# Kernel optimization log

Hardware: AMD Instinct MI355X
Metric: run time of the kernel (lower is better)

The kernel has to match this reference:

```python
import jax, jax.numpy as jnp
import numpy as np

TEMPERATURE = 0.1


def setup_inputs() -> dict:
    key = jax.random.key(0)
    k1, k2 = jax.random.split(key)
    N, D = 8192, 512
    embeddings = jax.random.normal(k1, (N, D), dtype=jnp.float32)
    labels = jax.random.randint(k2, (N,), 0, 16, dtype=jnp.int64)
    return {"embeddings": embeddings, "labels": labels}


def reference(embeddings, labels):
    # Vectorized SupCon: for each anchor i,
    #   +mean over positives j!=i of s_ij  -  logsumexp over all j!=i of s_ij
    # where s_ij = <e_i, e_j> / T. Final loss = -sum_i(...) / N * T.
    N = embeddings.shape[0]
    T = TEMPERATURE
    S = jnp.einsum('id,jd->ij', embeddings, embeddings) / T  # [N, N]
    eye = jnp.eye(N, dtype=bool)
    pos_mask = (labels[:, None] == labels[None, :]) & (~eye)  # positives, self excluded
    pos_counts = jnp.sum(pos_mask, axis=1)  # [N], assumed > 0 (every class has >=2 samples)
    pos_term = jnp.sum(jnp.where(pos_mask, S, 0.0), axis=1) / pos_counts
    neg_inf = jnp.array(-jnp.inf, dtype=S.dtype)
    lse = jax.nn.logsumexp(jnp.where(eye, neg_inf, S), axis=1)  # over j != i
    loss = jnp.sum(pos_term - lse)
    return -loss / N * T
```

## Files before the change

kernel.cpp:

```cpp
#include <hip/hip_runtime.h>
#include <stdint.h>

#define NROWS 8192
#define DIM   512
#define NPART 128

typedef __attribute__((ext_vector_type(8))) short short8;
typedef __attribute__((ext_vector_type(4))) float f32x4;
typedef unsigned int u32;

#define OFF_EBF   0u
#define OFF_X     8388608u
#define OFF_PM    8388608u
#define OFF_PL    12582912u
#define OFF_CLS   16777216u
#define OFF_CNT   16809984u
#define OFF_NRM   16810048u
#define OFF_BLK   16842816u

__device__ __forceinline__ void gload16(const void* g, void* l) {
  __builtin_amdgcn_global_load_lds((const __attribute__((address_space(1))) u32*)g,
                                   (__attribute__((address_space(3))) u32*)l, 16, 0, 0);
}

__device__ __forceinline__ unsigned short f2bf(float f) {
  u32 u = __float_as_uint(f);
  u32 r = (u + 0x7fffu + ((u >> 16) & 1u)) >> 16;
  return (unsigned short)r;
}

__global__ __launch_bounds__(256) void k_prep(const float* __restrict__ E,
                                              unsigned short* __restrict__ Ebf,
                                              float* __restrict__ nrm) {
  const int tid = threadIdx.x;
  const int lane = tid & 63;
  const int wid = tid >> 6;
  const int row = blockIdx.x * 4 + wid;
  const float4* src = (const float4*)(E + row * DIM + lane * 8);
  float4 v0 = src[0], v1 = src[1];
  float ns = v0.x*v0.x + v0.y*v0.y + v0.z*v0.z + v0.w*v0.w
           + v1.x*v1.x + v1.y*v1.y + v1.z*v1.z + v1.w*v1.w;
  u32 p0 = (u32)f2bf(v0.x) | ((u32)f2bf(v0.y) << 16);
  u32 p1 = (u32)f2bf(v0.z) | ((u32)f2bf(v0.w) << 16);
  u32 p2 = (u32)f2bf(v1.x) | ((u32)f2bf(v1.y) << 16);
  u32 p3 = (u32)f2bf(v1.z) | ((u32)f2bf(v1.w) << 16);
  *(uint4*)(Ebf + row * DIM + lane * 8) = make_uint4(p0, p1, p2, p3);
  #pragma unroll
  for (int s = 1; s < 64; s <<= 1) ns += __shfl_xor(ns, s);
  if (lane == 0) nrm[row] = ns;
}

__global__ __launch_bounds__(256) void k_cls(const float* __restrict__ E,
                                             const int* __restrict__ lab,
                                             float* __restrict__ Cpart,
                                             int* __restrict__ cnt) {
  __shared__ int lcnt[16];
  const int t = threadIdx.x;
  const int b = blockIdx.x;
  const int i0 = b * 32;
  if (t < 16) lcnt[t] = 0;
  __syncthreads();
  if (t < 32) atomicAdd(&lcnt[lab[i0 + t]], 1);
  float a0[16], a1[16];
  #pragma unroll
  for (int c = 0; c < 16; ++c) { a0[c] = 0.f; a1[c] = 0.f; }
  #pragma unroll 8
  for (int r = 0; r < 32; ++r) {
    const int lbl = lab[i0 + r];
    const float2 v = *(const float2*)(E + (i0 + r) * DIM + t * 2);
    #pragma unroll
    for (int c = 0; c < 16; ++c) {
      a0[c] += (c == lbl) ? v.x : 0.f;
      a1[c] += (c == lbl) ? v.y : 0.f;
    }
  }
  #pragma unroll
  for (int c = 0; c < 16; ++c)
    *(float2*)(Cpart + b * 8192 + c * DIM + t * 2) = make_float2(a0[c], a1[c]);
  __syncthreads();
  if (t < 16) atomicAdd(&cnt[t], lcnt[t]);
}

__global__ __launch_bounds__(256) void k_clsred(const float* __restrict__ Cpart,
                                                float* __restrict__ Cls) {
  const int idx = blockIdx.x * 256 + threadIdx.x;
  float s = 0.f;
  #pragma unroll 8
  for (int b = 0; b < 256; ++b) s += Cpart[b * 8192 + idx];
  Cls[idx] = s;
}

__global__ __launch_bounds__(256) void k_main(const unsigned short* __restrict__ Ebf,
                                              float* __restrict__ partM,
                                              float* __restrict__ partL) {
  const int jt = blockIdx.x;
  const int it = blockIdx.y;
  if (it > jt) return;

  __shared__ __align__(16) unsigned short As[128 * 64];
  __shared__ __align__(16) unsigned short Bs[128 * 64];

  const int tid  = threadIdx.x;
  const int lane = tid & 63;
  const int wid  = tid >> 6;
  const int wm   = wid >> 1;
  const int wn   = wid & 1;
  const int g    = lane >> 4;
  const int l15  = lane & 15;

  const int i0 = it * 128;
  const int j0 = jt * 128;

  const float C2 = 14.4269504088896f;

  int srow[4], selem[4];
  #pragma unroll
  for (int r = 0; r < 4; ++r) {
    const int D   = r * 4096 + tid * 16;
    const int row = D >> 7;
    const int cb  = (D >> 4) & 7;
    const int cs  = cb ^ (row & 7);
    srow[r]  = row;
    selem[r] = cs * 8;
  }

  f32x4 acc[4][4];
  #pragma unroll
  for (int a = 0; a < 4; ++a)
    #pragma unroll
    for (int b = 0; b < 4; ++b) {
      f32x4 z = {0.f, 0.f, 0.f, 0.f};
      acc[a][b] = z;
    }

  for (int kc = 0; kc < 8; ++kc) {
    #pragma unroll
    for (int r = 0; r < 4; ++r) {
      gload16(Ebf + (i0 + srow[r]) * DIM + kc * 64 + selem[r], &As[r * 2048 + tid * 8]);
      gload16(Ebf + (j0 + srow[r]) * DIM + kc * 64 + selem[r], &Bs[r * 2048 + tid * 8]);
    }
    __syncthreads();

    #pragma unroll
    for (int ks = 0; ks < 2; ++ks) {
      const int x = ((ks << 2) | g) ^ (l15 & 7);
      short8 av[4], bv[4];
      #pragma unroll
      for (int mf = 0; mf < 4; ++mf)
        av[mf] = *(const short8*)&As[(wm * 64 + mf * 16 + l15) * 64 + x * 8];
      #pragma unroll
      for (int nf = 0; nf < 4; ++nf)
        bv[nf] = *(const short8*)&Bs[(wn * 64 + nf * 16 + l15) * 64 + x * 8];
      #pragma unroll
      for (int mf = 0; mf < 4; ++mf)
        #pragma unroll
        for (int nf = 0; nf < 4; ++nf)
          acc[mf][nf] = __builtin_amdgcn_mfma_f32_16x16x32_bf16(av[mf], bv[nf], acc[mf][nf], 0, 0, 0);
    }
    __syncthreads();
  }

  const bool diagt = (it == jt);

  #pragma unroll
  for (int mf = 0; mf < 4; ++mf) {
    #pragma unroll
    for (int reg = 0; reg < 4; ++reg) {
      float v0 = acc[mf][0][reg];
      float v1 = acc[mf][1][reg];
      float v2 = acc[mf][2][reg];
      float v3 = acc[mf][3][reg];
      if (diagt) {
        const int rloc  = wm * 64 + mf * 16 + g * 4 + reg;
        const int cbase = wn * 64 + l15;
        v0 = (rloc == cbase)      ? -1e30f : v0;
        v1 = (rloc == cbase + 16) ? -1e30f : v1;
        v2 = (rloc == cbase + 32) ? -1e30f : v2;
        v3 = (rloc == cbase + 48) ? -1e30f : v3;
      }
      float m = fmaxf(fmaxf(v0, v1), fmaxf(v2, v3)) * C2;
      #pragma unroll
      for (int s = 1; s < 16; s <<= 1) m = fmaxf(m, __shfl_xor(m, s));
      float p = exp2f(__builtin_fmaf(v0, C2, -m)) + exp2f(__builtin_fmaf(v1, C2, -m))
              + exp2f(__builtin_fmaf(v2, C2, -m)) + exp2f(__builtin_fmaf(v3, C2, -m));
      #pragma unroll
      for (int s = 1; s < 16; s <<= 1) p += __shfl_xor(p, s);
      if (l15 == 0) {
        const int row = i0 + wm * 64 + mf * 16 + g * 4 + reg;
        partM[row * NPART + jt * 2 + wn] = m;
        partL[row * NPART + jt * 2 + wn] = p;
      }
    }
  }

  if (!diagt) {
    #pragma unroll
    for (int nf = 0; nf < 4; ++nf) {
      float m = -1e30f;
      #pragma unroll
      for (int mf = 0; mf < 4; ++mf)
        #pragma unroll
        for (int reg = 0; reg < 4; ++reg) m = fmaxf(m, acc[mf][nf][reg]);
      m *= C2;
      m = fmaxf(m, __shfl_xor(m, 16));
      m = fmaxf(m, __shfl_xor(m, 32));
      float p = 0.f;
      #pragma unroll
      for (int mf = 0; mf < 4; ++mf)
        #pragma unroll
        for (int reg = 0; reg < 4; ++reg)
          p += exp2f(__builtin_fmaf(acc[mf][nf][reg], C2, -m));
      p += __shfl_xor(p, 16);
      p += __shfl_xor(p, 32);
      if (g == 0) {
        const int row = j0 + wn * 64 + nf * 16 + l15;
        partM[row * NPART + it * 2 + wm] = m;
        partL[row * NPART + it * 2 + wm] = p;
      }
    }
  }
}

__global__ __launch_bounds__(256) void k_merge(const int* __restrict__ lab,
                                               const float* __restrict__ nrm,
                                               const float* __restrict__ partM,
                                               const float* __restrict__ partL,
                                               const int* __restrict__ cnt,
                                               float* __restrict__ blkout) {
  __shared__ float red[4];
  const int tid = threadIdx.x;
  const int lane = tid & 63;
  const int wid = tid >> 6;
  const int row = blockIdx.x * 4 + wid;

  float m1 = partM[row * NPART + lane];
  float l1 = partL[row * NPART + lane];
  const float m2 = partM[row * NPART + 64 + lane];
  const float l2 = partL[row * NPART + 64 + lane];
  float m = fmaxf(m1, m2);
  float l = l1 * exp2f(m1 - m) + l2 * exp2f(m2 - m);
  #pragma unroll
  for (int s = 1; s < 64; s <<= 1) {
    const float mo = __shfl_xor(m, s);
    const float lo = __shfl_xor(l, s);
    const float mn = fmaxf(m, mo);
    l = l * exp2f(m - mn) + lo * exp2f(mo - mn);
    m = mn;
  }
  if (lane == 0) {
    const float lse = 0.6931471805599453f * (m + log2f(l));
    const int lbl = lab[row];
    const float pc = (float)(cnt[lbl] - 1);
    red[wid] = -nrm[row] * 10.0f / pc - lse;
  }
  __syncthreads();
  if (tid == 0) blkout[blockIdx.x] = red[0] + red[1] + red[2] + red[3];
}

__global__ __launch_bounds__(256) void k_final(const float* __restrict__ blkout,
                                               const float* __restrict__ Cls,
                                               const int* __restrict__ cnt,
                                               float* __restrict__ out) {
  __shared__ float w[4];
  const int t = threadIdx.x;
  float s = 0.f;
  #pragma unroll
  for (int k = 0; k < 8; ++k) s += blkout[t + 256 * k];
  #pragma unroll
  for (int c = 0; c < 16; ++c) {
    const float2 v = *(const float2*)(Cls + c * DIM + t * 2);
    const float wc = 10.0f / (float)(cnt[c] - 1);
    s += wc * (v.x * v.x + v.y * v.y);
  }
  #pragma unroll
  for (int sh = 1; sh < 64; sh <<= 1) s += __shfl_xor(s, sh);
  if ((t & 63) == 0) w[t >> 6] = s;
  __syncthreads();
  if (t == 0) out[0] = (w[0] + w[1] + w[2] + w[3]) * (-0.1f / 8192.0f);
}

extern "C" void kernel_launch(void* const* d_in, const int* in_sizes, int n_in,
                              void* d_out, int out_size, void* d_ws, size_t ws_size,
                              hipStream_t stream) {
  (void)in_sizes; (void)n_in; (void)out_size; (void)ws_size;
  const float* E  = (const float*)d_in[0];
  const int* lab  = (const int*)d_in[1];
  char* ws = (char*)d_ws;
  unsigned short* Ebf = (unsigned short*)(ws + OFF_EBF);
  float* Cprt = (float*)(ws + OFF_X);
  float* pM   = (float*)(ws + OFF_PM);
  float* pL   = (float*)(ws + OFF_PL);
  float* Cls  = (float*)(ws + OFF_CLS);
  int*   cnt  = (int*)  (ws + OFF_CNT);
  float* nrm  = (float*)(ws + OFF_NRM);
  float* blk  = (float*)(ws + OFF_BLK);

  hipMemsetAsync(ws + OFF_CNT, 0, 64, stream);

  k_prep  <<<NROWS / 4, 256, 0, stream>>>(E, Ebf, nrm);
  k_cls   <<<256, 256, 0, stream>>>(E, lab, Cprt, cnt);
  k_clsred<<<32, 256, 0, stream>>>(Cprt, Cls);
  dim3 grid(64, 64);
  k_main  <<<grid, 256, 0, stream>>>(Ebf, pM, pL);
  k_merge <<<NROWS / 4, 256, 0, stream>>>(lab, nrm, pM, pL, cnt, blk);
  k_final <<<1, 256, 0, stream>>>(blk, Cls, cnt, (float*)d_out);
}
```

Measured before the change: 208.9 us.

## Drop LDS staging in GEMM, compact triangular grid, use LDS atomics for class sums

The main Gram kernel no longer stages tiles in LDS. Each wave loads its bf16 fragments straight from global memory into registers, which removes the barriers and LDS traffic. The 64x64 grid, where half the blocks exited early, becomes a 65x32 grid that maps onto the upper triangle of tiles exactly, so no launched block is wasted. The class-sum kernel now accumulates in shared memory with atomics over 64 rows per block and launches half as many partial blocks. The trade-off is that operand reuse now depends on L1/L2 caching instead of LDS, and uncoalesced direct loads with LDS atomic contention may cost more than they save.

```diff
diff --git a/kernel.cpp b/kernel.cpp
--- a/kernel.cpp
+++ b/kernel.cpp
@@ -17,11 +17,6 @@
 #define OFF_CNT   16809984u
 #define OFF_NRM   16810048u
 #define OFF_BLK   16842816u
-
-__device__ __forceinline__ void gload16(const void* g, void* l) {
-  __builtin_amdgcn_global_load_lds((const __attribute__((address_space(1))) u32*)g,
-                                   (__attribute__((address_space(3))) u32*)l, 16, 0, 0);
-}
 
 __device__ __forceinline__ unsigned short f2bf(float f) {
   u32 u = __float_as_uint(f);
@@ -54,30 +49,23 @@
                                              const int* __restrict__ lab,
                                              float* __restrict__ Cpart,
                                              int* __restrict__ cnt) {
+  __shared__ float lcls[16 * DIM];
   __shared__ int lcnt[16];
   const int t = threadIdx.x;
   const int b = blockIdx.x;
-  const int i0 = b * 32;
+  const int i0 = b * 64;
+  for (int k = t; k < 16 * DIM; k += 256) lcls[k] = 0.f;
   if (t < 16) lcnt[t] = 0;
   __syncthreads();
-  if (t < 32) atomicAdd(&lcnt[lab[i0 + t]], 1);
-  float a0[16], a1[16];
-  #pragma unroll
-  for (int c = 0; c < 16; ++c) { a0[c] = 0.f; a1[c] = 0.f; }
-  #pragma unroll 8
-  for (int r = 0; r < 32; ++r) {
+  if (t < 64) atomicAdd(&lcnt[lab[i0 + t]], 1);
+  for (int r = 0; r < 64; ++r) {
     const int lbl = lab[i0 + r];
     const float2 v = *(const float2*)(E + (i0 + r) * DIM + t * 2);
-    #pragma unroll
-    for (int c = 0; c < 16; ++c) {
-      a0[c] += (c == lbl) ? v.x : 0.f;
-      a1[c] += (c == lbl) ? v.y : 0.f;
-    }
-  }
-  #pragma unroll
-  for (int c = 0; c < 16; ++c)
-    *(float2*)(Cpart + b * 8192 + c * DIM + t * 2) = make_float2(a0[c], a1[c]);
-  __syncthreads();
+    atomicAdd(&lcls[lbl * DIM + t * 2],     v.x);
+    atomicAdd(&lcls[lbl * DIM + t * 2 + 1], v.y);
+  }
+  __syncthreads();
+  for (int k = t; k < 16 * DIM; k += 256) Cpart[b * 8192 + k] = lcls[k];
   if (t < 16) atomicAdd(&cnt[t], lcnt[t]);
 }
 
@@ -86,19 +74,18 @@
   const int idx = blockIdx.x * 256 + threadIdx.x;
   float s = 0.f;
   #pragma unroll 8
-  for (int b = 0; b < 256; ++b) s += Cpart[b * 8192 + idx];
+  for (int b = 0; b < 128; ++b) s += Cpart[b * 8192 + idx];
   Cls[idx] = s;
 }
 
 __global__ __launch_bounds__(256) void k_main(const unsigned short* __restrict__ Ebf,
                                               float* __restrict__ partM,
                                               float* __restrict__ partL) {
-  const int jt = blockIdx.x;
-  const int it = blockIdx.y;
-  if (it > jt) return;
-
-  __shared__ __align__(16) unsigned short As[128 * 64];
-  __shared__ __align__(16) unsigned short Bs[128 * 64];
+  const int x = blockIdx.x;
+  const int y = blockIdx.y;
+  int IT, JT;
+  if (x < 64 - y) { IT = y;      JT = y + x; }
+  else            { IT = 63 - y; JT = x - 1; }
 
   const int tid  = threadIdx.x;
   const int lane = tid & 63;
@@ -108,59 +95,58 @@
   const int g    = lane >> 4;
   const int l15  = lane & 15;
 
-  const int i0 = it * 128;
-  const int j0 = jt * 128;
+  const int a = IT * 2 + wm;
+  const int b = JT * 2 + wn;
+  const bool diagblk = (IT == JT);
+  const bool diag64  = (a == b);
 
   const float C2 = 14.4269504088896f;
 
-  int srow[4], selem[4];
-  #pragma unroll
-  for (int r = 0; r < 4; ++r) {
-    const int D   = r * 4096 + tid * 16;
-    const int row = D >> 7;
-    const int cb  = (D >> 4) & 7;
-    const int cs  = cb ^ (row & 7);
-    srow[r]  = row;
-    selem[r] = cs * 8;
-  }
+  const unsigned short* pa0 = Ebf + (a * 64 + l15) * DIM + g * 8;
+  const unsigned short* pb0 = Ebf + (b * 64 + l15) * DIM + g * 8;
+  const unsigned short* pa1 = pa0 + 16 * DIM;
+  const unsigned short* pa2 = pa0 + 32 * DIM;
+  const unsigned short* pa3 = pa0 + 48 * DIM;
+  const unsigned short* pb1 = pb0 + 16 * DIM;
+  const unsigned short* pb2 = pb0 + 32 * DIM;
+  const unsigned short* pb3 = pb0 + 48 * DIM;
 
   f32x4 acc[4][4];
   #pragma unroll
-  for (int a = 0; a < 4; ++a)
+  for (int i = 0; i < 4; ++i)
     #pragma unroll
-    for (int b = 0; b < 4; ++b) {
+    for (int j = 0; j < 4; ++j) {
       f32x4 z = {0.f, 0.f, 0.f, 0.f};
-      acc[a][b] = z;
+      acc[i][j] = z;
     }
 
-  for (int kc = 0; kc < 8; ++kc) {
-    #pragma unroll
-    for (int r = 0; r < 4; ++r) {
-      gload16(Ebf + (i0 + srow[r]) * DIM + kc * 64 + selem[r], &As[r * 2048 + tid * 8]);
-      gload16(Ebf + (j0 + srow[r]) * DIM + kc * 64 + selem[r], &Bs[r * 2048 + tid * 8]);
-    }
-    __syncthreads();
-
-    #pragma unroll
-    for (int ks = 0; ks < 2; ++ks) {
-      const int x = ((ks << 2) | g) ^ (l15 & 7);
-      short8 av[4], bv[4];
-      #pragma unroll
-      for (int mf = 0; mf < 4; ++mf)
-        av[mf] = *(const short8*)&As[(wm * 64 + mf * 16 + l15) * 64 + x * 8];
-      #pragma unroll
-      for (int nf = 0; nf < 4; ++nf)
-        bv[nf] = *(const short8*)&Bs[(wn * 64 + nf * 16 + l15) * 64 + x * 8];
-      #pragma unroll
-      for (int mf = 0; mf < 4; ++mf)
-        #pragma unroll
-        for (int nf = 0; nf < 4; ++nf)
-          acc[mf][nf] = __builtin_amdgcn_mfma_f32_16x16x32_bf16(av[mf], bv[nf], acc[mf][nf], 0, 0, 0);
-    }
-    __syncthreads();
-  }
-
-  const bool diagt = (it == jt);
+  #pragma unroll 4
+  for (int ks = 0; ks < 16; ++ks) {
+    short8 av0 = *(const short8*)(pa0 + ks * 32);
+    short8 av1 = *(const short8*)(pa1 + ks * 32);
+    short8 av2 = *(const short8*)(pa2 + ks * 32);
+    short8 av3 = *(const short8*)(pa3 + ks * 32);
+    short8 bv0 = *(const short8*)(pb0 + ks * 32);
+    short8 bv1 = *(const short8*)(pb1 + ks * 32);
+    short8 bv2 = *(const short8*)(pb2 + ks * 32);
+    short8 bv3 = *(const short8*)(pb3 + ks * 32);
+    acc[0][0] = __builtin_amdgcn_mfma_f32_16x16x32_bf16(av0, bv0, acc[0][0], 0, 0, 0);
+    acc[0][1] = __builtin_amdgcn_mfma_f32_16x16x32_bf16(av0, bv1, acc[0][1], 0, 0, 0);
+    acc[0][2] = __builtin_amdgcn_mfma_f32_16x16x32_bf16(av0, bv2, acc[0][2], 0, 0, 0);
+    acc[0][3] = __builtin_amdgcn_mfma_f32_16x16x32_bf16(av0, bv3, acc[0][3], 0, 0, 0);
+    acc[1][0] = __builtin_amdgcn_mfma_f32_16x16x32_bf16(av1, bv0, acc[1][0], 0, 0, 0);
+    acc[1][1] = __builtin_amdgcn_mfma_f32_16x16x32_bf16(av1, bv1, acc[1][1], 0, 0, 0);
+    acc[1][2] = __builtin_amdgcn_mfma_f32_16x16x32_bf16(av1, bv2, acc[1][2], 0, 0, 0);
+    acc[1][3] = __builtin_amdgcn_mfma_f32_16x16x32_bf16(av1, bv3, acc[1][3], 0, 0, 0);
+    acc[2][0] = __builtin_amdgcn_mfma_f32_16x16x32_bf16(av2, bv0, acc[2][0], 0, 0, 0);
+    acc[2][1] = __builtin_amdgcn_mfma_f32_16x16x32_bf16(av2, bv1, acc[2][1], 0, 0, 0);
+    acc[2][2] = __builtin_amdgcn_mfma_f32_16x16x32_bf16(av2, bv2, acc[2][2], 0, 0, 0);
+    acc[2][3] = __builtin_amdgcn_mfma_f32_16x16x32_bf16(av2, bv3, acc[2][3], 0, 0, 0);
+    acc[3][0] = __builtin_amdgcn_mfma_f32_16x16x32_bf16(av3, bv0, acc[3][0], 0, 0, 0);
+    acc[3][1] = __builtin_amdgcn_mfma_f32_16x16x32_bf16(av3, bv1, acc[3][1], 0, 0, 0);
+    acc[3][2] = __builtin_amdgcn_mfma_f32_16x16x32_bf16(av3, bv2, acc[3][2], 0, 0, 0);
+    acc[3][3] = __builtin_amdgcn_mfma_f32_16x16x32_bf16(av3, bv3, acc[3][3], 0, 0, 0);
+  }
 
   #pragma unroll
   for (int mf = 0; mf < 4; ++mf) {
@@ -170,13 +156,12 @@
       float v1 = acc[mf][1][reg];
       float v2 = acc[mf][2][reg];
       float v3 = acc[mf][3][reg];
-      if (diagt) {
-        const int rloc  = wm * 64 + mf * 16 + g * 4 + reg;
-        const int cbase = wn * 64 + l15;
-        v0 = (rloc == cbase)      ? -1e30f : v0;
-        v1 = (rloc == cbase + 16) ? -1e30f : v1;
-        v2 = (rloc == cbase + 32) ? -1e30f : v2;
-        v3 = (rloc == cbase + 48) ? -1e30f : v3;
+      if (diag64) {
+        const int rloc = mf * 16 + g * 4 + reg;
+        v0 = (rloc == l15)      ? -1e30f : v0;
+        v1 = (rloc == 16 + l15) ? -1e30f : v1;
+        v2 = (rloc == 32 + l15) ? -1e30f : v2;
+        v3 = (rloc == 48 + l15) ? -1e30f : v3;
       }
       float m = fmaxf(fmaxf(v0, v1), fmaxf(v2, v3)) * C2;
       #pragma unroll
@@ -186,14 +171,14 @@
       #pragma unroll
       for (int s = 1; s < 16; s <<= 1) p += __shfl_xor(p, s);
       if (l15 == 0) {
-        const int row = i0 + wm * 64 + mf * 16 + g * 4 + reg;
-        partM[row * NPART + jt * 2 + wn] = m;
-        partL[row * NPART + jt * 2 + wn] = p;
+        const int row = a * 64 + mf * 16 + g * 4 + reg;
+        partM[row * NPART + b] = m;
+        partL[row * NPART + b] = p;
       }
     }
   }
 
-  if (!diagt) {
+  if (!diagblk) {
     #pragma unroll
     for (int nf = 0; nf < 4; ++nf) {
       float m = -1e30f;
@@ -213,9 +198,9 @@
       p += __shfl_xor(p, 16);
       p += __shfl_xor(p, 32);
       if (g == 0) {
-        const int row = j0 + wn * 64 + nf * 16 + l15;
-        partM[row * NPART + it * 2 + wm] = m;
-        partL[row * NPART + it * 2 + wm] = p;
+        const int row = b * 64 + nf * 16 + l15;
+        partM[row * NPART + a] = m;
+        partL[row * NPART + a] = p;
       }
     }
   }
@@ -298,9 +283,9 @@
   hipMemsetAsync(ws + OFF_CNT, 0, 64, stream);
 
   k_prep  <<<NROWS / 4, 256, 0, stream>>>(E, Ebf, nrm);
-  k_cls   <<<256, 256, 0, stream>>>(E, lab, Cprt, cnt);
+  k_cls   <<<128, 256, 0, stream>>>(E, lab, Cprt, cnt);
   k_clsred<<<32, 256, 0, stream>>>(Cprt, Cls);
-  dim3 grid(64, 64);
+  dim3 grid(65, 32);
   k_main  <<<grid, 256, 0, stream>>>(Ebf, pM, pL);
   k_merge <<<NROWS / 4, 256, 0, stream>>>(lab, nrm, pM, pL, cnt, blk);
   k_final <<<1, 256, 0, stream>>>(blk, Cls, cnt, (float*)d_out);
```

Measured after the change: 289.8 us. 1.39x slower.

## Balance triangular tile schedule in main kernel and build class sums from bf16

Applied to the files above, without the earlier changes.

The main kernel used to launch a full 64x64 grid and return early from the lower-triangle blocks. It now launches 1024 blocks. Each block walks a folded pair of triangle rows, so every block handles two or three tiles, which balances work and removes the idle launches. Separately, the class-sum kernel now reads the bf16 copy and accumulates with LDS float atomics instead of register select chains. That halves the global reads but lowers class-sum precision to bf16 and adds atomic contention in shared memory.

```diff
diff --git a/kernel.cpp b/kernel.cpp
--- a/kernel.cpp
+++ b/kernel.cpp
@@ -50,34 +50,27 @@
   if (lane == 0) nrm[row] = ns;
 }
 
-__global__ __launch_bounds__(256) void k_cls(const float* __restrict__ E,
+__global__ __launch_bounds__(256) void k_cls(const unsigned short* __restrict__ Ebf,
                                              const int* __restrict__ lab,
                                              float* __restrict__ Cpart,
                                              int* __restrict__ cnt) {
+  __shared__ float lcls[16 * DIM];
   __shared__ int lcnt[16];
   const int t = threadIdx.x;
   const int b = blockIdx.x;
   const int i0 = b * 32;
+  for (int k = t; k < 16 * DIM; k += 256) lcls[k] = 0.f;
   if (t < 16) lcnt[t] = 0;
   __syncthreads();
   if (t < 32) atomicAdd(&lcnt[lab[i0 + t]], 1);
-  float a0[16], a1[16];
-  #pragma unroll
-  for (int c = 0; c < 16; ++c) { a0[c] = 0.f; a1[c] = 0.f; }
-  #pragma unroll 8
   for (int r = 0; r < 32; ++r) {
     const int lbl = lab[i0 + r];
-    const float2 v = *(const float2*)(E + (i0 + r) * DIM + t * 2);
-    #pragma unroll
-    for (int c = 0; c < 16; ++c) {
-      a0[c] += (c == lbl) ? v.x : 0.f;
-      a1[c] += (c == lbl) ? v.y : 0.f;
-    }
-  }
-  #pragma unroll
-  for (int c = 0; c < 16; ++c)
-    *(float2*)(Cpart + b * 8192 + c * DIM + t * 2) = make_float2(a0[c], a1[c]);
+    const ushort2 v = *(const ushort2*)(Ebf + (i0 + r) * DIM + t * 2);
+    atomicAdd(&lcls[lbl * DIM + t * 2],     __uint_as_float((u32)v.x << 16));
+    atomicAdd(&lcls[lbl * DIM + t * 2 + 1], __uint_as_float((u32)v.y << 16));
+  }
   __syncthreads();
+  for (int k = t; k < 16 * DIM; k += 256) Cpart[b * 8192 + k] = lcls[k];
   if (t < 16) atomicAdd(&cnt[t], lcnt[t]);
 }
 
@@ -93,12 +86,14 @@
 __global__ __launch_bounds__(256) void k_main(const unsigned short* __restrict__ Ebf,
                                               float* __restrict__ partM,
                                               float* __restrict__ partL) {
-  const int jt = blockIdx.x;
-  const int it = blockIdx.y;
-  if (it > jt) return;
-
   __shared__ __align__(16) unsigned short As[128 * 64];
   __shared__ __align__(16) unsigned short Bs[128 * 64];
+
+  const int bid = blockIdx.x;
+  const int p = bid & 31;
+  const int c = bid >> 5;
+  const int nq  = (c == 0) ? 3 : 2;
+  const int off = (c == 0) ? 0 : (2 * c + 1);
 
   const int tid  = threadIdx.x;
   const int lane = tid & 63;
@@ -108,9 +103,6 @@
   const int g    = lane >> 4;
   const int l15  = lane & 15;
 
-  const int i0 = it * 128;
-  const int j0 = jt * 128;
-
   const float C2 = 14.4269504088896f;
 
   int srow[4], selem[4];
@@ -124,98 +116,106 @@
     selem[r] = cs * 8;
   }
 
-  f32x4 acc[4][4];
-  #pragma unroll
-  for (int a = 0; a < 4; ++a)
+  for (int qq = 0; qq < nq; ++qq) {
+    const int q = off + qq;
+    const int len1 = 64 - p;
+    const int it = (q < len1) ? p : 63 - p;
+    const int jt = (q < len1) ? p + q : (63 - p) + (q - len1);
+    const int i0 = it * 128;
+    const int j0 = jt * 128;
+    const bool diagt = (it == jt);
+
+    f32x4 acc[4][4];
     #pragma unroll
-    for (int b = 0; b < 4; ++b) {
-      f32x4 z = {0.f, 0.f, 0.f, 0.f};
-      acc[a][b] = z;
+    for (int a = 0; a < 4; ++a)
+      #pragma unroll
+      for (int b = 0; b < 4; ++b) {
+        f32x4 z = {0.f, 0.f, 0.f, 0.f};
+        acc[a][b] = z;
+      }
+
+    for (int kc = 0; kc < 8; ++kc) {
+      #pragma unroll
+      for (int r = 0; r < 4; ++r) {
+        gload16(Ebf + (i0 + srow[r]) * DIM + kc * 64 + selem[r], &As[r * 2048 + tid * 8]);
+        gload16(Ebf + (j0 + srow[r]) * DIM + kc * 64 + selem[r], &Bs[r * 2048 + tid * 8]);
+      }
+      __syncthreads();
+
+      #pragma unroll
+      for (int ks = 0; ks < 2; ++ks) {
+        const int x = ((ks << 2) | g) ^ (l15 & 7);
+        short8 av[4], bv[4];
+        #pragma unroll
+        for (int mf = 0; mf < 4; ++mf)
+          av[mf] = *(const short8*)&As[(wm * 64 + mf * 16 + l15) * 64 + x * 8];
+        #pragma unroll
+        for (int nf = 0; nf < 4; ++nf)
+          bv[nf] = *(const short8*)&Bs[(wn * 64 + nf * 16 + l15) * 64 + x * 8];
+        #pragma unroll
+        for (int mf = 0; mf < 4; ++mf)
+          #pragma unroll
+          for (int nf = 0; nf < 4; ++nf)
+            acc[mf][nf] = __builtin_amdgcn_mfma_f32_16x16x32_bf16(av[mf], bv[nf], acc[mf][nf], 0, 0, 0);
+      }
+      __syncthreads();
     }
 
-  for (int kc = 0; kc < 8; ++kc) {
     #pragma unroll
-    for (int r = 0; r < 4; ++r) {
-      gload16(Ebf + (i0 + srow[r]) * DIM + kc * 64 + selem[r], &As[r * 2048 + tid * 8]);
-      gload16(Ebf + (j0 + srow[r]) * DIM + kc * 64 + selem[r], &Bs[r * 2048 + tid * 8]);
+    for (int mf = 0; mf < 4; ++mf) {
+      #pragma unroll
+      for (int reg = 0; reg < 4; ++reg) {
+        float v0 = acc[mf][0][reg];
+        float v1 = acc[mf][1][reg];
+        float v2 = acc[mf][2][reg];
+        float v3 = acc[mf][3][reg];
+        if (diagt) {
+          const int rloc  = wm * 64 + mf * 16 + g * 4 + reg;
+          const int cbase = wn * 64 + l15;
+          v0 = (rloc == cbase)      ? -1e30f : v0;
+          v1 = (rloc == cbase + 16) ? -1e30f : v1;
+          v2 = (rloc == cbase + 32) ? -1e30f : v2;
+          v3 = (rloc == cbase + 48) ? -1e30f : v3;
+        }
+        float m = fmaxf(fmaxf(v0, v1), fmaxf(v2, v3)) * C2;
+        #pragma unroll
+        for (int s = 1; s < 16; s <<= 1) m = fmaxf(m, __shfl_xor(m, s));
+        float pp = exp2f(__builtin_fmaf(v0, C2, -m)) + exp2f(__builtin_fmaf(v1, C2, -m))
+                 + exp2f(__builtin_fmaf(v2, C2, -m)) + exp2f(__builtin_fmaf(v3, C2, -m));
+        #pragma unroll
+        for (int s = 1; s < 16; s <<= 1) pp += __shfl_xor(pp, s);
+        if (l15 == 0) {
+          const int row = i0 + wm * 64 + mf * 16 + g * 4 + reg;
+          partM[row * NPART + jt * 2 + wn] = m;
+          partL[row * NPART + jt * 2 + wn] = pp;
+        }
+      }
     }
-    __syncthreads();
-
-    #pragma unroll
-    for (int ks = 0; ks < 2; ++ks) {
-      const int x = ((ks << 2) | g) ^ (l15 & 7);
-      short8 av[4], bv[4];
-      #pragma unroll
-      for (int mf = 0; mf < 4; ++mf)
-        av[mf] = *(const short8*)&As[(wm * 64 + mf * 16 + l15) * 64 + x * 8];
-      #pragma unroll
-      for (int nf = 0; nf < 4; ++nf)
-        bv[nf] = *(const short8*)&Bs[(wn * 64 + nf * 16 + l15) * 64 + x * 8];
-      #pragma unroll
-      for (int mf = 0; mf < 4; ++mf)
-        #pragma unroll
-        for (int nf = 0; nf < 4; ++nf)
-          acc[mf][nf] = __builtin_amdgcn_mfma_f32_16x16x32_bf16(av[mf], bv[nf], acc[mf][nf], 0, 0, 0);
-    }
-    __syncthreads();
-  }
-
-  const bool diagt = (it == jt);
-
-  #pragma unroll
-  for (int mf = 0; mf < 4; ++mf) {
-    #pragma unroll
-    for (int reg = 0; reg < 4; ++reg) {
-      float v0 = acc[mf][0][reg];
-      float v1 = acc[mf][1][reg];
-      float v2 = acc[mf][2][reg];
-      float v3 = acc[mf][3][reg];
-      if (diagt) {
-        const int rloc  = wm * 64 + mf * 16 + g * 4 + reg;
-        const int cbase = wn * 64 + l15;
-        v0 = (rloc == cbase)      ? -1e30f : v0;
-        v1 = (rloc == cbase + 16) ? -1e30f : v1;
-        v2 = (rloc == cbase + 32) ? -1e30f : v2;
-        v3 = (rloc == cbase + 48) ? -1e30f : v3;
-      }
-      float m = fmaxf(fmaxf(v0, v1), fmaxf(v2, v3)) * C2;
-      #pragma unroll
-      for (int s = 1; s < 16; s <<= 1) m = fmaxf(m, __shfl_xor(m, s));
-      float p = exp2f(__builtin_fmaf(v0, C2, -m)) + exp2f(__builtin_fmaf(v1, C2, -m))
-              + exp2f(__builtin_fmaf(v2, C2, -m)) + exp2f(__builtin_fmaf(v3, C2, -m));
-      #pragma unroll
-      for (int s = 1; s < 16; s <<= 1) p += __shfl_xor(p, s);
-      if (l15 == 0) {
-        const int row = i0 + wm * 64 + mf * 16 + g * 4 + reg;
-        partM[row * NPART + jt * 2 + wn] = m;
-        partL[row * NPART + jt * 2 + wn] = p;
-      }
-    }
-  }
-
-  if (!diagt) {
-    #pragma unroll
-    for (int nf = 0; nf < 4; ++nf) {
-      float m = -1e30f;
-      #pragma unroll
-      for (int mf = 0; mf < 4; ++mf)
-        #pragma unroll
-        for (int reg = 0; reg < 4; ++reg) m = fmaxf(m, acc[mf][nf][reg]);
-      m *= C2;
-      m = fmaxf(m, __shfl_xor(m, 16));
-      m = fmaxf(m, __shfl_xor(m, 32));
-      float p = 0.f;
-      #pragma unroll
-      for (int mf = 0; mf < 4; ++mf)
-        #pragma unroll
-        for (int reg = 0; reg < 4; ++reg)
-          p += exp2f(__builtin_fmaf(acc[mf][nf][reg], C2, -m));
-      p += __shfl_xor(p, 16);
-      p += __shfl_xor(p, 32);
-      if (g == 0) {
-        const int row = j0 + wn * 64 + nf * 16 + l15;
-        partM[row * NPART + it * 2 + wm] = m;
-        partL[row * NPART + it * 2 + wm] = p;
+
+    if (!diagt) {
+      #pragma unroll
+      for (int nf = 0; nf < 4; ++nf) {
+        float m = -1e30f;
+        #pragma unroll
+        for (int mf = 0; mf < 4; ++mf)
+          #pragma unroll
+          for (int reg = 0; reg < 4; ++reg) m = fmaxf(m, acc[mf][nf][reg]);
+        m *= C2;
+        m = fmaxf(m, __shfl_xor(m, 16));
+        m = fmaxf(m, __shfl_xor(m, 32));
+        float pp = 0.f;
+        #pragma unroll
+        for (int mf = 0; mf < 4; ++mf)
+          #pragma unroll
+          for (int reg = 0; reg < 4; ++reg)
+            pp += exp2f(__builtin_fmaf(acc[mf][nf][reg], C2, -m));
+        pp += __shfl_xor(pp, 16);
+        pp += __shfl_xor(pp, 32);
+        if (g == 0) {
+          const int row = j0 + wn * 64 + nf * 16 + l15;
+          partM[row * NPART + it * 2 + wm] = m;
+          partL[row * NPART + it * 2 + wm] = pp;
+        }
       }
     }
   }
@@ -298,10 +298,9 @@
   hipMemsetAsync(ws + OFF_CNT, 0, 64, stream);
 
   k_prep  <<<NROWS / 4, 256, 0, stream>>>(E, Ebf, nrm);
-  k_cls   <<<256, 256, 0, stream>>>(E, lab, Cprt, cnt);
+  k_cls   <<<256, 256, 0, stream>>>(Ebf, lab, Cprt, cnt);
   k_clsred<<<32, 256, 0, stream>>>(Cprt, Cls);
-  dim3 grid(64, 64);
-  k_main  <<<grid, 256, 0, stream>>>(Ebf, pM, pL);
+  k_main  <<<1024, 256, 0, stream>>>(Ebf, pM, pL);
   k_merge <<<NROWS / 4, 256, 0, stream>>>(lab, nrm, pM, pL, cnt, blk);
   k_final <<<1, 256, 0, stream>>>(blk, Cls, cnt, (float*)d_out);
 }
```

Result: faster. 202.4 us (-3.1%).
